# Kernel optimization log

Hardware: AMD Instinct MI355X
Metric: run time of the kernel (lower is better)

## Reference

```python
import jax, jax.numpy as jnp
import numpy as np

BS, N, DIM, HEADS = 4, 2048, 512, 8
HEAD_DIM = DIM // HEADS
SCALE = HEAD_DIM ** 0.5
NEG = -1000000.0


def setup_inputs() -> dict:
    key = jax.random.key(0)
    ks = jax.random.split(key, 6)
    x = jax.random.normal(ks[0], (BS, N, DIM), dtype=jnp.float32)
    mask = jax.random.randint(ks[1], (BS, N), 0, 2, dtype=jnp.int32)
    s = 1.0 / np.sqrt(DIM)
    Wq = jax.random.normal(ks[2], (DIM, DIM), dtype=jnp.float32) * s
    Wk = jax.random.normal(ks[3], (DIM, DIM), dtype=jnp.float32) * s
    Wv = jax.random.normal(ks[4], (DIM, DIM), dtype=jnp.float32) * s
    Wo = jax.random.normal(ks[5], (DIM, DIM), dtype=jnp.float32) * s
    return {"x": x, "Wq": Wq, "Wk": Wk, "Wv": Wv, "Wo": Wo, "mask": mask}


def reference(x, Wq, Wk, Wv, Wo, mask):
    # q,k,v: (bs, n, dim) -> (bs, h, n, d)
    def split_heads(t):
        return t.reshape(BS, N, HEADS, HEAD_DIM).transpose(0, 2, 1, 3)
    q = split_heads(x @ Wq.T)
    k = split_heads(x @ Wk.T)
    v = split_heads(x @ Wv.T)
    # scores: (bs, h, n, n)
    scores = jnp.einsum('bhqd,bhkd->bhqk', q, k) / SCALE
    # key-padding mask broadcast over heads and query positions
    keep = (mask == 1)[:, None, None, :]  # (bs,1,1,n)
    scores = jnp.where(keep, scores, NEG)
    attn = jax.nn.softmax(scores, axis=-1)
    out = jnp.einsum('bhqk,bhkd->bhqd', attn, v)
    out = out.transpose(0, 2, 1, 3).reshape(BS, N, DIM)
    return out @ Wo.T
```

## Files before the change

kernel.cpp:

```cpp
#include <hip/hip_runtime.h>
#include <hip/hip_bf16.h>

#define BS 4
#define SEQ 2048
#define DIM 512
#define HEADS 8
#define HD 64
#define ROWS (BS*SEQ)
#define SCL2E 0.1803368801111244f
#define NEGB (-1.4426950408889634e6f)

typedef __attribute__((ext_vector_type(8))) short bf16x8;
typedef __attribute__((ext_vector_type(4))) short bf16x4;
typedef __attribute__((ext_vector_type(4))) float floatx4;
typedef unsigned short u16;
typedef unsigned int u32;

__device__ __forceinline__ u16 f2bf(float f) {
    union { float f; unsigned u; } v; v.f = f;
    unsigned r = v.u + 0x7fff + ((v.u >> 16) & 1);
    return (u16)(r >> 16);
}

__device__ __forceinline__ unsigned pack2bf(float a, float b) {
#if __has_builtin(__builtin_amdgcn_cvt_pk_bf16_f32)
    typedef __attribute__((ext_vector_type(2))) __bf16 bf2;
    union { bf2 v; unsigned u; } cv;
    cv.v = __builtin_amdgcn_cvt_pk_bf16_f32(a, b);
    return cv.u;
#else
    return (unsigned)f2bf(a) | ((unsigned)f2bf(b) << 16);
#endif
}

__device__ __forceinline__ float fexp2(float x) {
#if __has_builtin(__builtin_amdgcn_exp2f)
    return __builtin_amdgcn_exp2f(x);
#else
    return __expf(x * 0.6931471805599453f);
#endif
}

__device__ __forceinline__ void gload16(const u16* g, u16* l) {
    __builtin_amdgcn_global_load_lds(
        (const __attribute__((address_space(1))) u32*)g,
        (__attribute__((address_space(3))) u32*)l, 16, 0, 0);
}

__global__ __launch_bounds__(256) void convert_all(
    const float* __restrict__ x, const float* __restrict__ Wq,
    const float* __restrict__ Wk, const float* __restrict__ Wv,
    const float* __restrict__ Wo, const int* __restrict__ mask,
    u16* __restrict__ xb, u16* __restrict__ wqb,
    u16* __restrict__ wkb, u16* __restrict__ wvb,
    u16* __restrict__ wob, float* __restrict__ biasf)
{
    int i = blockIdx.x * 256 + threadIdx.x;
    if (i < 1048576 + 262144) {
        const float* src; u16* dst; int off;
        if (i < 1048576) { src = x; dst = xb; off = i; }
        else {
            int j = i - 1048576; int seg = j >> 16; off = j & 65535;
            src = seg == 0 ? Wq : seg == 1 ? Wk : seg == 2 ? Wv : Wo;
            dst = seg == 0 ? wqb : seg == 1 ? wkb : seg == 2 ? wvb : wob;
        }
        float4 v = ((const float4*)src)[off];
        ushort4 o;
        o.x = f2bf(v.x); o.y = f2bf(v.y); o.z = f2bf(v.z); o.w = f2bf(v.w);
        ((ushort4*)dst)[off] = o;
    } else {
        int jb = i - 1310720;
        int4 mv = ((const int4*)mask)[jb];
        float4 bo;
        bo.x = (mv.x == 1) ? 0.f : NEGB;
        bo.y = (mv.y == 1) ? 0.f : NEGB;
        bo.z = (mv.z == 1) ? 0.f : NEGB;
        bo.w = (mv.w == 1) ? 0.f : NEGB;
        ((float4*)biasf)[jb] = bo;
    }
}

__global__ __launch_bounds__(256, 3) void gemm_qkv_fused(
    const u16* __restrict__ A, const u16* __restrict__ Wcat,
    u16* __restrict__ Oq, u16* __restrict__ Okf, u16* __restrict__ Ovf)
{
    __shared__ u16 ldsA[8192];
    __shared__ u16 ldsB[8192];

    int flat = blockIdx.y * 12 + blockIdx.x;
    int c  = flat & 7, s = flat >> 3;
    int bx = s % 12;
    int by = (s / 12) * 8 + c;
    int n0 = bx * 128;
    int m0 = by * 128;
    int tid = threadIdx.x;
    int w = tid >> 6, lane = tid & 63, quad = lane >> 4, l16 = lane & 15;
    int mo = (w & 1) * 64, no = (w >> 1) * 64;
    int l7 = l16 & 7;

    int sr = lane >> 3, sc = lane & 7, gc = sc ^ sr;
    const u16* gA0 = A    + (long)(m0 + sr) * DIM + gc * 8;
    const u16* gB0 = Wcat + (long)(n0 + sr) * DIM + gc * 8;

    floatx4 acc[4][4];
    #pragma unroll
    for (int mt = 0; mt < 4; mt++)
        #pragma unroll
        for (int nt = 0; nt < 4; nt++) acc[mt][nt] = (floatx4){0.f,0.f,0.f,0.f};

    for (int k0 = 0; k0 < DIM; k0 += 64) {
        #pragma unroll
        for (int i = 0; i < 4; i++) {
            int ch = w * 4 + i;
            gload16(gA0 + (long)ch * 8 * DIM + k0, &ldsA[ch * 512]);
            gload16(gB0 + (long)ch * 8 * DIM + k0, &ldsB[ch * 512]);
        }
        __syncthreads();

        #pragma unroll
        for (int kc = 0; kc < 2; kc++) {
            int swz = ((kc * 4 + quad) ^ l7) * 8;
            bf16x8 af[4], bf[4];
            #pragma unroll
            for (int t4 = 0; t4 < 4; t4++) {
                af[t4] = *(const bf16x8*)&ldsA[(mo + t4*16 + l16) * 64 + swz];
                bf[t4] = *(const bf16x8*)&ldsB[(no + t4*16 + l16) * 64 + swz];
            }
            #pragma unroll
            for (int mt = 0; mt < 4; mt++)
                #pragma unroll
                for (int nt = 0; nt < 4; nt++)
                    acc[mt][nt] = __builtin_amdgcn_mfma_f32_16x16x32_bf16(
                        af[mt], bf[nt], acc[mt][nt], 0, 0, 0);
        }
        __syncthreads();
    }

    int seg = n0 >> 9;
    if (seg == 0) {
        #pragma unroll
        for (int mt = 0; mt < 4; mt++)
            #pragma unroll
            for (int nt = 0; nt < 4; nt++)
                #pragma unroll
                for (int r = 0; r < 4; r++) {
                    int row = m0 + mo + mt*16 + quad*4 + r;
                    int col9 = (n0 + no + nt*16 + l16) & 511;
                    int b = row >> 11, n = row & 2047, h = col9 >> 6, d = col9 & 63;
                    Oq[(((long)(b * HEADS + h) * SEQ + n) << 6) + d] = f2bf(acc[mt][nt][r]);
                }
    } else if (seg == 1) {
        #pragma unroll
        for (int mt = 0; mt < 4; mt++)
            #pragma unroll
            for (int nt = 0; nt < 4; nt++)
                #pragma unroll
                for (int r = 0; r < 4; r++) {
                    int row = m0 + mo + mt*16 + quad*4 + r;
                    int col9 = (n0 + no + nt*16 + l16) & 511;
                    int b = row >> 11, keyn = row & 2047, h = col9 >> 6, dd = col9 & 63;
                    int kt = keyn >> 6, ntk = (keyn >> 4) & 3, l16k = keyn & 15;
                    int g = dd >> 5, quadk = (dd >> 3) & 3, j = dd & 7;
                    long offv = ((long)((b*HEADS + h)*32 + kt) << 12)
                              + ((ntk*2 + g) << 9) + ((quadk*16 + l16k) << 3) + j;
                    Okf[offv] = f2bf(acc[mt][nt][r] * SCL2E);
                }
    } else {
        #pragma unroll
        for (int mt = 0; mt < 4; mt++)
            #pragma unroll
            for (int nt = 0; nt < 4; nt++) {
                int rowb = m0 + mo + mt*16 + quad*4;
                int col9 = (n0 + no + nt*16 + l16) & 511;
                int b = rowb >> 11, keyn = rowb & 2047, h = col9 >> 6;
                int tile = (keyn >> 6) & 31;
                long offv = ((long)((b*HEADS + h)*32 + tile) << 12)
                          + ((long)(mt >> 1) << 11) + (nt << 9)
                          + ((quad*16 + l16) << 3) + ((mt & 1) << 2);
                ushort4 st;
                st.x = f2bf(acc[mt][nt][0]); st.y = f2bf(acc[mt][nt][1]);
                st.z = f2bf(acc[mt][nt][2]); st.w = f2bf(acc[mt][nt][3]);
                *(ushort4*)&Ovf[offv] = st;
            }
    }
}

__global__ __launch_bounds__(256, 2) void flash_attn(
    const u16* __restrict__ Q, const u16* __restrict__ Kf,
    const u16* __restrict__ Vf, const float* __restrict__ biasf,
    u16* __restrict__ ctx)
{
    __shared__ float red[4352];

    int bx = blockIdx.x;
    int cx = bx & 7, sx = bx >> 3;
    int gg = ((sx >> 5) << 3) | cx;
    int qi = sx & 31;
    int q0 = qi * 64;
    int h  = gg & 7;
    int b  = gg >> 3;
    int bh = b * HEADS + h;

    int tid = threadIdx.x;
    int w = tid >> 6, lane = tid & 63, quad = lane >> 4, l16 = lane & 15;

    bf16x8 qb[4][2];
    #pragma unroll
    for (int nt = 0; nt < 4; nt++) {
        const u16* qp = Q + ((long)bh * SEQ + q0 + nt*16 + l16) * HD + quad * 8;
        qb[nt][0] = *(const bf16x8*)(qp);
        qb[nt][1] = *(const bf16x8*)(qp + 32);
    }

    const u16* Kw = Kf + ((long)bh << 17) + w*2048 + lane*8;
    const u16* Vw = Vf + ((long)bh << 17) + w*2048 + lane*8;
    const float* bw = biasf + b * SEQ + w*32 + quad*4;

    short one_s = (l16 == 0) ? (short)0x3F80 : (short)0;
    bf16x8 ones8 = { one_s, one_s, one_s, one_s, one_s, one_s, one_s, one_s };

    bf16x8 k00 = *(const bf16x8*)(Kw);
    bf16x8 k01 = *(const bf16x8*)(Kw + 512);
    bf16x8 k10 = *(const bf16x8*)(Kw + 1024);
    bf16x8 k11 = *(const bf16x8*)(Kw + 1536);
    bf16x8 vb0 = *(const bf16x8*)(Vw);
    bf16x8 vb1 = *(const bf16x8*)(Vw + 512);
    bf16x8 vb2 = *(const bf16x8*)(Vw + 1024);
    bf16x8 vb3 = *(const bf16x8*)(Vw + 1536);
    float4 bv0 = *(const float4*)(bw);
    float4 bv1 = *(const float4*)(bw + 16);

    floatx4 o[4][4];
    floatx4 o5[4];
    #pragma unroll
    for (int nt = 0; nt < 4; nt++) {
        #pragma unroll
        for (int ct = 0; ct < 4; ct++) o[nt][ct] = (floatx4){0.f,0.f,0.f,0.f};
        o5[nt] = (floatx4){0.f,0.f,0.f,0.f};
    }

    #pragma unroll 2
    for (int it = 0; it < 16; it++) {
        bf16x8 k00n=k00, k01n=k01, k10n=k10, k11n=k11;
        bf16x8 vb0n=vb0, vb1n=vb1, vb2n=vb2, vb3n=vb3;
        float4 bv0n=bv0, bv1n=bv1;
        if (it < 15) {
            const u16* kp = Kw + (long)(it+1)*8192;
            const u16* vp = Vw + (long)(it+1)*8192;
            k00n = *(const bf16x8*)(kp);
            k01n = *(const bf16x8*)(kp + 512);
            k10n = *(const bf16x8*)(kp + 1024);
            k11n = *(const bf16x8*)(kp + 1536);
            vb0n = *(const bf16x8*)(vp);
            vb1n = *(const bf16x8*)(vp + 512);
            vb2n = *(const bf16x8*)(vp + 1024);
            vb3n = *(const bf16x8*)(vp + 1536);
            bv0n = *(const float4*)(bw + (it+1)*128);
            bv1n = *(const float4*)(bw + (it+1)*128 + 16);
        }

        #pragma unroll
        for (int nt = 0; nt < 4; nt++) {
            floatx4 s0, s1;
            s0[0] = bv0.x; s0[1] = bv0.y; s0[2] = bv0.z; s0[3] = bv0.w;
            s1[0] = bv1.x; s1[1] = bv1.y; s1[2] = bv1.z; s1[3] = bv1.w;
            __builtin_amdgcn_s_setprio(1);
            s0 = __builtin_amdgcn_mfma_f32_16x16x32_bf16(k00, qb[nt][0], s0, 0, 0, 0);
            s0 = __builtin_amdgcn_mfma_f32_16x16x32_bf16(k01, qb[nt][1], s0, 0, 0, 0);
            s1 = __builtin_amdgcn_mfma_f32_16x16x32_bf16(k10, qb[nt][0], s1, 0, 0, 0);
            s1 = __builtin_amdgcn_mfma_f32_16x16x32_bf16(k11, qb[nt][1], s1, 0, 0, 0);
            __builtin_amdgcn_s_setprio(0);
            float p0 = fexp2(s0[0]);
            float p1 = fexp2(s0[1]);
            float p2 = fexp2(s0[2]);
            float p3 = fexp2(s0[3]);
            float p4 = fexp2(s1[0]);
            float p5 = fexp2(s1[1]);
            float p6 = fexp2(s1[2]);
            float p7 = fexp2(s1[3]);
            union { bf16x8 v; unsigned u[4]; } pu;
            pu.u[0] = pack2bf(p0, p1);
            pu.u[1] = pack2bf(p2, p3);
            pu.u[2] = pack2bf(p4, p5);
            pu.u[3] = pack2bf(p6, p7);
            __builtin_amdgcn_s_setprio(1);
            o[nt][0] = __builtin_amdgcn_mfma_f32_16x16x32_bf16(pu.v, vb0, o[nt][0], 0, 0, 0);
            o[nt][1] = __builtin_amdgcn_mfma_f32_16x16x32_bf16(pu.v, vb1, o[nt][1], 0, 0, 0);
            o[nt][2] = __builtin_amdgcn_mfma_f32_16x16x32_bf16(pu.v, vb2, o[nt][2], 0, 0, 0);
            o[nt][3] = __builtin_amdgcn_mfma_f32_16x16x32_bf16(pu.v, vb3, o[nt][3], 0, 0, 0);
            o5[nt] = __builtin_amdgcn_mfma_f32_16x16x32_bf16(pu.v, ones8, o5[nt], 0, 0, 0);
            __builtin_amdgcn_s_setprio(0);
        }

        k00 = k00n; k01 = k01n; k10 = k10n; k11 = k11n;
        vb0 = vb0n; vb1 = vb1n; vb2 = vb2n; vb3 = vb3n;
        bv0 = bv0n; bv1 = bv1n;
    }

    __syncthreads();
    float* ldsf = red;
    floatx4* ldsv = (floatx4*)red;

    if (l16 == 0) {
        #pragma unroll
        for (int nt = 0; nt < 4; nt++)
            #pragma unroll
            for (int r = 0; r < 4; r++)
                ldsf[4096 + w*64 + nt*16 + quad*4 + r] = o5[nt][r];
    }
    __syncthreads();

    #pragma unroll
    for (int i2 = 1; i2 < 4; i2++) {
        int tslot = (w + i2) & 3;
        #pragma unroll
        for (int nt = 0; nt < 4; nt++)
            if (nt == tslot) {
                #pragma unroll
                for (int ct = 0; ct < 4; ct++)
                    ldsv[nt*256 + ct*64 + lane] = o[nt][ct];
            }
        __syncthreads();
        #pragma unroll
        for (int nt = 0; nt < 4; nt++)
            if (nt == w) {
                #pragma unroll
                for (int ct = 0; ct < 4; ct++) {
                    floatx4 v = ldsv[nt*256 + ct*64 + lane];
                    o[nt][ct] += v;
                }
            }
        __syncthreads();
    }

    #pragma unroll
    for (int nt = 0; nt < 4; nt++) {
        if (nt != w) continue;
        float inv[4];
        #pragma unroll
        for (int r = 0; r < 4; r++) {
            int q = w*16 + quad*4 + r;
            float sden = ldsf[4096 + q] + ldsf[4096 + 64 + q]
                       + ldsf[4096 + 128 + q] + ldsf[4096 + 192 + q];
            inv[r] = 1.0f / sden;
        }
        #pragma unroll
        for (int ct = 0; ct < 4; ct++) {
            int col = h * HD + ct*16 + l16;
            long rb = (long)(b * SEQ + q0 + w*16 + quad*4);
            #pragma unroll
            for (int r = 0; r < 4; r++)
                ctx[(rb + r) * DIM + col] = f2bf(o[nt][ct][r] * inv[r]);
        }
    }
}

__global__ __launch_bounds__(256, 4) void gemm_proj(
    const u16* __restrict__ A, const u16* __restrict__ Bt,
    float* __restrict__ Out)
{
    __shared__ u16 ldsA[4096];
    __shared__ u16 ldsB[4096];

    int n0 = blockIdx.x * 64;
    int m0 = blockIdx.y * 64;
    int tid = threadIdx.x;
    int w = tid >> 6, lane = tid & 63, quad = lane >> 4, l16 = lane & 15;
    int l7 = l16 & 7;

    int sr = lane >> 3, sc = lane & 7, gc = sc ^ sr;
    const u16* gA0 = A  + (long)(m0 + sr) * DIM + gc * 8;
    const u16* gB0 = Bt + (long)(n0 + sr) * DIM + gc * 8;

    floatx4 acc[4];
    #pragma unroll
    for (int nt = 0; nt < 4; nt++) acc[nt] = (floatx4){0.f,0.f,0.f,0.f};

    for (int k0 = 0; k0 < DIM; k0 += 64) {
        #pragma unroll
        for (int i = 0; i < 2; i++) {
            int ch = 2*w + i;
            gload16(gA0 + (long)ch * 8 * DIM + k0, &ldsA[ch * 512]);
            gload16(gB0 + (long)ch * 8 * DIM + k0, &ldsB[ch * 512]);
        }
        __syncthreads();

        #pragma unroll
        for (int kc = 0; kc < 2; kc++) {
            int swz = ((kc * 4 + quad) ^ l7) * 8;
            bf16x8 af = *(const bf16x8*)&ldsA[(w*16 + l16) * 64 + swz];
            #pragma unroll
            for (int nt = 0; nt < 4; nt++) {
                bf16x8 bfv = *(const bf16x8*)&ldsB[(nt*16 + l16) * 64 + swz];
                acc[nt] = __builtin_amdgcn_mfma_f32_16x16x32_bf16(
                    af, bfv, acc[nt], 0, 0, 0);
            }
        }
        __syncthreads();
    }

    #pragma unroll
    for (int nt = 0; nt < 4; nt++)
        #pragma unroll
        for (int r = 0; r < 4; r++) {
            int row = m0 + w*16 + quad*4 + r;
            int col = n0 + nt*16 + l16;
            Out[(long)row * DIM + col] = acc[nt][r];
        }
}

extern "C" void kernel_launch(void* const* d_in, const int* in_sizes, int n_in,
                              void* d_out, int out_size, void* d_ws, size_t ws_size,
                              hipStream_t stream) {
    const float* x  = (const float*)d_in[0];
    const float* Wq = (const float*)d_in[1];
    const float* Wk = (const float*)d_in[2];
    const float* Wv = (const float*)d_in[3];
    const float* Wo = (const float*)d_in[4];
    const int* mask = (const int*)d_in[5];
    float* out = (float*)d_out;

    char* ws = (char*)d_ws;
    size_t off = 0;
    u16* xb  = (u16*)(ws + off); off += (size_t)ROWS * DIM * 2;
    u16* wqb = (u16*)(ws + off); off += (size_t)DIM * DIM * 2;
    u16* wkb = (u16*)(ws + off); off += (size_t)DIM * DIM * 2;
    u16* wvb = (u16*)(ws + off); off += (size_t)DIM * DIM * 2;
    u16* wob = (u16*)(ws + off); off += (size_t)DIM * DIM * 2;
    u16* Qh  = (u16*)(ws + off); off += (size_t)ROWS * DIM * 2;
    u16* Kfr = (u16*)(ws + off); off += (size_t)ROWS * DIM * 2;
    u16* Vfr = (u16*)(ws + off); off += (size_t)ROWS * DIM * 2;
    u16* ctx = (u16*)(ws + off); off += (size_t)ROWS * DIM * 2;
    float* biasf = (float*)(ws + off); off += (size_t)BS * SEQ * 4;

    convert_all<<<5128, 256, 0, stream>>>(x, Wq, Wk, Wv, Wo, mask,
                                          xb, wqb, wkb, wvb, wob, biasf);
    gemm_qkv_fused<<<dim3(12, 64), 256, 0, stream>>>(xb, wqb, Qh, Kfr, Vfr);
    flash_attn<<<BS * HEADS * (SEQ / 64), 256, 0, stream>>>(Qh, Kfr, Vfr, biasf, ctx);
    gemm_proj<<<dim3(8, 128), 256, 0, stream>>>(ctx, wob, out);

    (void)in_sizes; (void)n_in; (void)out_size; (void)ws_size;
}
```

Baseline: 157.1 us.

## Shrink QKV GEMM tile to 64x128 with per-wave 16-row strips

The fused QKV projection now uses 64x128 tiles, double the grid rows (12x128 blocks), and halves the A tile in LDS. Each wave computes one 16-row strip across all 128 columns, and occupancy hint rises to 4 blocks per SM. The intent is more blocks to fill the GPU and better latency hiding, at the cost of reloading the B tile for twice as many blocks and a lower MFMA-to-LDS-load ratio. The V-store layout arithmetic is rederived for the new per-wave mapping.

```diff
diff --git a/kernel.cpp b/kernel.cpp
--- a/kernel.cpp
+++ b/kernel.cpp
@@ -80,11 +80,11 @@
     }
 }
 
-__global__ __launch_bounds__(256, 3) void gemm_qkv_fused(
+__global__ __launch_bounds__(256, 4) void gemm_qkv_fused(
     const u16* __restrict__ A, const u16* __restrict__ Wcat,
     u16* __restrict__ Oq, u16* __restrict__ Okf, u16* __restrict__ Ovf)
 {
-    __shared__ u16 ldsA[8192];
+    __shared__ u16 ldsA[4096];
     __shared__ u16 ldsB[8192];
 
     int flat = blockIdx.y * 12 + blockIdx.x;
@@ -92,27 +92,28 @@
     int bx = s % 12;
     int by = (s / 12) * 8 + c;
     int n0 = bx * 128;
-    int m0 = by * 128;
+    int m0 = by * 64;
     int tid = threadIdx.x;
     int w = tid >> 6, lane = tid & 63, quad = lane >> 4, l16 = lane & 15;
-    int mo = (w & 1) * 64, no = (w >> 1) * 64;
     int l7 = l16 & 7;
 
     int sr = lane >> 3, sc = lane & 7, gc = sc ^ sr;
     const u16* gA0 = A    + (long)(m0 + sr) * DIM + gc * 8;
     const u16* gB0 = Wcat + (long)(n0 + sr) * DIM + gc * 8;
 
-    floatx4 acc[4][4];
-    #pragma unroll
-    for (int mt = 0; mt < 4; mt++)
-        #pragma unroll
-        for (int nt = 0; nt < 4; nt++) acc[mt][nt] = (floatx4){0.f,0.f,0.f,0.f};
+    floatx4 acc[8];
+    #pragma unroll
+    for (int nt = 0; nt < 8; nt++) acc[nt] = (floatx4){0.f,0.f,0.f,0.f};
 
     for (int k0 = 0; k0 < DIM; k0 += 64) {
         #pragma unroll
+        for (int i = 0; i < 2; i++) {
+            int ch = 2*w + i;
+            gload16(gA0 + (long)ch * 8 * DIM + k0, &ldsA[ch * 512]);
+        }
+        #pragma unroll
         for (int i = 0; i < 4; i++) {
-            int ch = w * 4 + i;
-            gload16(gA0 + (long)ch * 8 * DIM + k0, &ldsA[ch * 512]);
+            int ch = 4*w + i;
             gload16(gB0 + (long)ch * 8 * DIM + k0, &ldsB[ch * 512]);
         }
         __syncthreads();
@@ -120,18 +121,13 @@
         #pragma unroll
         for (int kc = 0; kc < 2; kc++) {
             int swz = ((kc * 4 + quad) ^ l7) * 8;
-            bf16x8 af[4], bf[4];
-            #pragma unroll
-            for (int t4 = 0; t4 < 4; t4++) {
-                af[t4] = *(const bf16x8*)&ldsA[(mo + t4*16 + l16) * 64 + swz];
-                bf[t4] = *(const bf16x8*)&ldsB[(no + t4*16 + l16) * 64 + swz];
-            }
-            #pragma unroll
-            for (int mt = 0; mt < 4; mt++)
-                #pragma unroll
-                for (int nt = 0; nt < 4; nt++)
-                    acc[mt][nt] = __builtin_amdgcn_mfma_f32_16x16x32_bf16(
-                        af[mt], bf[nt], acc[mt][nt], 0, 0, 0);
+            bf16x8 af = *(const bf16x8*)&ldsA[(w*16 + l16) * 64 + swz];
+            #pragma unroll
+            for (int nt = 0; nt < 8; nt++) {
+                bf16x8 bfv = *(const bf16x8*)&ldsB[(nt*16 + l16) * 64 + swz];
+                acc[nt] = __builtin_amdgcn_mfma_f32_16x16x32_bf16(
+                    af, bfv, acc[nt], 0, 0, 0);
+            }
         }
         __syncthreads();
     }
@@ -139,49 +135,46 @@
     int seg = n0 >> 9;
     if (seg == 0) {
         #pragma unroll
-        for (int mt = 0; mt < 4; mt++)
-            #pragma unroll
-            for (int nt = 0; nt < 4; nt++)
-                #pragma unroll
-                for (int r = 0; r < 4; r++) {
-                    int row = m0 + mo + mt*16 + quad*4 + r;
-                    int col9 = (n0 + no + nt*16 + l16) & 511;
-                    int b = row >> 11, n = row & 2047, h = col9 >> 6, d = col9 & 63;
-                    Oq[(((long)(b * HEADS + h) * SEQ + n) << 6) + d] = f2bf(acc[mt][nt][r]);
-                }
+        for (int nt = 0; nt < 8; nt++)
+            #pragma unroll
+            for (int r = 0; r < 4; r++) {
+                int row = m0 + w*16 + quad*4 + r;
+                int col9 = (n0 + nt*16 + l16) & 511;
+                int b = row >> 11, n = row & 2047, h = col9 >> 6, d = col9 & 63;
+                Oq[(((long)(b * HEADS + h) * SEQ + n) << 6) + d] = f2bf(acc[nt][r]);
+            }
     } else if (seg == 1) {
         #pragma unroll
-        for (int mt = 0; mt < 4; mt++)
-            #pragma unroll
-            for (int nt = 0; nt < 4; nt++)
-                #pragma unroll
-                for (int r = 0; r < 4; r++) {
-                    int row = m0 + mo + mt*16 + quad*4 + r;
-                    int col9 = (n0 + no + nt*16 + l16) & 511;
-                    int b = row >> 11, keyn = row & 2047, h = col9 >> 6, dd = col9 & 63;
-                    int kt = keyn >> 6, ntk = (keyn >> 4) & 3, l16k = keyn & 15;
-                    int g = dd >> 5, quadk = (dd >> 3) & 3, j = dd & 7;
-                    long offv = ((long)((b*HEADS + h)*32 + kt) << 12)
-                              + ((ntk*2 + g) << 9) + ((quadk*16 + l16k) << 3) + j;
-                    Okf[offv] = f2bf(acc[mt][nt][r] * SCL2E);
-                }
+        for (int nt = 0; nt < 8; nt++)
+            #pragma unroll
+            for (int r = 0; r < 4; r++) {
+                int row = m0 + w*16 + quad*4 + r;
+                int col9 = (n0 + nt*16 + l16) & 511;
+                int b = row >> 11, keyn = row & 2047, h = col9 >> 6, dd = col9 & 63;
+                int kt = keyn >> 6, ntk = (keyn >> 4) & 3, l16k = keyn & 15;
+                int g = dd >> 5, quadk = (dd >> 3) & 3, j = dd & 7;
+                long offv = ((long)((b*HEADS + h)*32 + kt) << 12)
+                          + ((ntk*2 + g) << 9) + ((quadk*16 + l16k) << 3) + j;
+                Okf[offv] = f2bf(acc[nt][r] * SCL2E);
+            }
     } else {
         #pragma unroll
-        for (int mt = 0; mt < 4; mt++)
-            #pragma unroll
-            for (int nt = 0; nt < 4; nt++) {
-                int rowb = m0 + mo + mt*16 + quad*4;
-                int col9 = (n0 + no + nt*16 + l16) & 511;
-                int b = rowb >> 11, keyn = rowb & 2047, h = col9 >> 6;
-                int tile = (keyn >> 6) & 31;
-                long offv = ((long)((b*HEADS + h)*32 + tile) << 12)
-                          + ((long)(mt >> 1) << 11) + (nt << 9)
-                          + ((quad*16 + l16) << 3) + ((mt & 1) << 2);
-                ushort4 st;
-                st.x = f2bf(acc[mt][nt][0]); st.y = f2bf(acc[mt][nt][1]);
-                st.z = f2bf(acc[mt][nt][2]); st.w = f2bf(acc[mt][nt][3]);
-                *(ushort4*)&Ovf[offv] = st;
-            }
+        for (int nt = 0; nt < 8; nt++) {
+            int rowb = m0 + w*16 + quad*4;
+            int col9 = (n0 + nt*16 + l16) & 511;
+            int b = rowb >> 11, keyn = rowb & 2047, h = col9 >> 6;
+            int dd = col9 & 63;
+            int tile = (keyn >> 6) & 31;
+            int pair = (keyn >> 5) & 1, sbit = (keyn >> 4) & 1;
+            int ct = dd >> 4;
+            long offv = ((long)((b*HEADS + h)*32 + tile) << 12)
+                      + ((long)pair << 11) + (ct << 9)
+                      + ((quad*16 + l16) << 3) + (sbit << 2);
+            ushort4 st;
+            st.x = f2bf(acc[nt][0]); st.y = f2bf(acc[nt][1]);
+            st.z = f2bf(acc[nt][2]); st.w = f2bf(acc[nt][3]);
+            *(ushort4*)&Ovf[offv] = st;
+        }
     }
 }
 
@@ -435,7 +428,7 @@
 
     convert_all<<<5128, 256, 0, stream>>>(x, Wq, Wk, Wv, Wo, mask,
                                           xb, wqb, wkb, wvb, wob, biasf);
-    gemm_qkv_fused<<<dim3(12, 64), 256, 0, stream>>>(xb, wqb, Qh, Kfr, Vfr);
+    gemm_qkv_fused<<<dim3(12, 128), 256, 0, stream>>>(xb, wqb, Qh, Kfr, Vfr);
     flash_attn<<<BS * HEADS * (SEQ / 64), 256, 0, stream>>>(Qh, Kfr, Vfr, biasf, ctx);
     gemm_proj<<<dim3(8, 128), 256, 0, stream>>>(ctx, wob, out);
 
```

After: 158.9 us. About the same (+1.1%).
